# Optimization experiments

Measured on AMD Instinct MI355X. Metric: run time of the kernel, lower is better.

The kernel has to match this reference:

```python
import jax, jax.numpy as jnp
import numpy as np

B, S, D, H = 2, 2048, 2048, 16
HD = D // H
RESIDUAL_SCALE = 1.0
EPS = 1e-6


def setup_inputs() -> dict:
    key = jax.random.key(0)
    ks = jax.random.split(key, 6)
    x = jax.random.normal(ks[0], (B, S, D), jnp.float32)
    # rotary tables: emb = cat(freqs, freqs), shape [S, HD]
    inv_freq = 1.0 / (10000.0 ** (jnp.arange(0, HD, 2, dtype=jnp.float32) / HD))
    t = jnp.arange(S, dtype=jnp.float32)
    freqs = jnp.einsum('s,f->sf', t, inv_freq)
    emb = jnp.concatenate([freqs, freqs], axis=-1)
    cos, sin = jnp.cos(emb), jnp.sin(emb)
    sc = 0.02
    w_qkv = jax.random.normal(ks[1], (3 * D, D), jnp.float32) * sc
    w_out = jax.random.normal(ks[2], (D, D), jnp.float32) * sc
    w_fc1 = jax.random.normal(ks[3], (4 * D, D), jnp.float32) * sc
    w_fc2 = jax.random.normal(ks[4], (D, 4 * D), jnp.float32) * sc
    g1 = jnp.ones((D,), jnp.float32)
    g2 = jnp.ones((D,), jnp.float32)
    return {'x': x, 'cos': cos, 'sin': sin, 'g1': g1, 'g2': g2,
            'w_qkv': w_qkv, 'w_out': w_out, 'w_fc1': w_fc1, 'w_fc2': w_fc2}


def _rmsnorm(x, g):
    xf = x.astype(jnp.float32)
    norm = jnp.sqrt(jnp.mean(xf * xf, axis=-1, keepdims=True) + EPS)
    return g * (xf / norm)


def _rotate_half(x):
    x1, x2 = jnp.split(x, 2, axis=-1)
    return jnp.concatenate([-x2, x1], axis=-1)


def _rope(t, cos, sin):
    # t: [B, S, H, HD]; cos/sin: [S, HD]
    c = cos[None, :, None, :]
    s = sin[None, :, None, :]
    return t * c + _rotate_half(t) * s


def reference(x, cos, sin, g1, g2, w_qkv, w_out, w_fc1, w_fc2):
    b, s, d = x.shape
    x_skip = x
    h = _rmsnorm(x, g1)
    qkv = (h @ w_qkv.T).reshape(b, s, 3, H, HD)
    q = _rope(qkv[:, :, 0], cos, sin)
    k = _rope(qkv[:, :, 1], cos, sin)
    v = qkv[:, :, 2]  # rotary is identity on v
    scale = 1.0 / jnp.sqrt(jnp.asarray(HD, dtype=q.dtype))
    scores = jnp.einsum('bqhd,bkhd->bhqk', q, k) * scale
    causal = jnp.triu(jnp.ones((s, s), dtype=bool), k=1)
    scores = jnp.where(causal[None, None], -jnp.inf, scores)
    attn = jax.nn.softmax(scores, axis=-1)
    o = jnp.einsum('bhqk,bkhd->bqhd', attn, v).reshape(b, s, d)
    x = x_skip + RESIDUAL_SCALE * (o @ w_out.T)
    x_skip = x
    h = _rmsnorm(x, g2)
    h = jax.nn.gelu(h @ w_fc1.T, approximate=True) @ w_fc2.T
    return x_skip + RESIDUAL_SCALE * h
```

## Files before the change

kernel.cpp:

```cpp
#include <hip/hip_runtime.h>
#include <stdint.h>

typedef unsigned short u16;
typedef u16 u16x4 __attribute__((ext_vector_type(4)));
typedef u16 u16x8 __attribute__((ext_vector_type(8)));
typedef __bf16 bf16x8 __attribute__((ext_vector_type(8)));
typedef float f32x4 __attribute__((ext_vector_type(4)));
typedef float f32x16 __attribute__((ext_vector_type(16)));

#define MFMA16 __builtin_amdgcn_mfma_f32_16x16x32_bf16
#define MFMA32 __builtin_amdgcn_mfma_f32_32x32x16_bf16

static __device__ __forceinline__ float b2f(u16 u) {
    union { unsigned int i; float f; } v; v.i = ((unsigned int)u) << 16; return v.f;
}
static __device__ __forceinline__ u16 f2b(float f) {
    union { float f; unsigned int i; } v; v.f = f;
    unsigned int r = (v.i + 0x7fffu + ((v.i >> 16) & 1u)) >> 16;
    return (u16)r;
}
static __device__ __forceinline__ unsigned pk2(float lo, float hi) {
    union { __bf16 b[2]; unsigned u; } t;
    t.b[0] = (__bf16)lo; t.b[1] = (__bf16)hi; return t.u;
}
static __device__ __forceinline__ void gload_lds16(const void* g, void* l) {
    __builtin_amdgcn_global_load_lds((__attribute__((address_space(1))) void*)g,
                                     (__attribute__((address_space(3))) void*)l,
                                     16, 0, 0);
}

__global__ __launch_bounds__(256) void cvt4_k(const float* __restrict__ s0,
                                              const float* __restrict__ s1,
                                              const float* __restrict__ s2,
                                              const float* __restrict__ s3,
                                              u16* __restrict__ out) {
    long i = ((long)blockIdx.x * 256 + threadIdx.x) * 4;
    const float* src; long off;
    if (i < 12582912)      { src = s0; off = i; }
    else if (i < 16777216) { src = s1; off = i - 12582912; }
    else if (i < 33554432) { src = s2; off = i - 16777216; }
    else                   { src = s3; off = i - 33554432; }
    float4 v = *(const float4*)(src + off);
    u16x4 o; o[0] = f2b(v.x); o[1] = f2b(v.y); o[2] = f2b(v.z); o[3] = f2b(v.w);
    *(u16x4*)(out + i) = o;
}

__global__ __launch_bounds__(256) void addred_k(float* __restrict__ xout,
                                                const float* __restrict__ p0,
                                                const float* __restrict__ p1) {
    long i = ((long)blockIdx.x * 256 + threadIdx.x) * 4;
    float4 a = *(const float4*)(xout + i);
    float4 b = *(const float4*)(p0 + i);
    float4 c = *(const float4*)(p1 + i);
    a.x += b.x + c.x; a.y += b.y + c.y; a.z += b.z + c.z; a.w += b.w + c.w;
    *(float4*)(xout + i) = a;
}

__global__ __launch_bounds__(256) void addrednorm_k(float* xout,
                                                    const float* __restrict__ x,
                                                    const float* p0,
                                                    const float* __restrict__ p1,
                                                    const float* __restrict__ g,
                                                    u16* __restrict__ out) {
    const long row = blockIdx.x;
    const int tid = threadIdx.x;
    const long base = row * 2048;
    float4 a = *(const float4*)(x + base + tid * 4);
    float4 b = *(const float4*)(p0 + base + tid * 4);
    float4 c = *(const float4*)(p1 + base + tid * 4);
    a.x += b.x + c.x; a.y += b.y + c.y; a.z += b.z + c.z; a.w += b.w + c.w;
    float4 a2 = *(const float4*)(x + base + 1024 + tid * 4);
    float4 b2 = *(const float4*)(p0 + base + 1024 + tid * 4);
    float4 c2 = *(const float4*)(p1 + base + 1024 + tid * 4);
    a2.x += b2.x + c2.x; a2.y += b2.y + c2.y;
    a2.z += b2.z + c2.z; a2.w += b2.w + c2.w;
    *(float4*)(xout + base + tid * 4) = a;
    *(float4*)(xout + base + 1024 + tid * 4) = a2;
    float ss = a.x*a.x + a.y*a.y + a.z*a.z + a.w*a.w
             + a2.x*a2.x + a2.y*a2.y + a2.z*a2.z + a2.w*a2.w;
    #pragma unroll
    for (int d = 1; d < 64; d <<= 1) ss += __shfl_xor(ss, d);
    __shared__ float red[4];
    if ((tid & 63) == 0) red[tid >> 6] = ss;
    __syncthreads();
    float tot = red[0] + red[1] + red[2] + red[3];
    float rinv = rsqrtf(tot * (1.0f / 2048.0f) + 1e-6f);
    float4 g0 = *(const float4*)(g + tid * 4);
    float4 g1 = *(const float4*)(g + 1024 + tid * 4);
    u16x4 o0, o1;
    o0[0] = f2b(a.x * g0.x * rinv); o0[1] = f2b(a.y * g0.y * rinv);
    o0[2] = f2b(a.z * g0.z * rinv); o0[3] = f2b(a.w * g0.w * rinv);
    o1[0] = f2b(a2.x * g1.x * rinv); o1[1] = f2b(a2.y * g1.y * rinv);
    o1[2] = f2b(a2.z * g1.z * rinv); o1[3] = f2b(a2.w * g1.w * rinv);
    *(u16x4*)(out + base + tid * 4) = o0;
    *(u16x4*)(out + base + 1024 + tid * 4) = o1;
}

__global__ __launch_bounds__(256) void rmsnorm_k(const float* __restrict__ x,
                                                 const float* __restrict__ g,
                                                 u16* __restrict__ out) {
    const long row = blockIdx.x;
    const int tid = threadIdx.x;
    const float* xr = x + row * 2048;
    float4 a = *(const float4*)(xr + tid * 4);
    float4 b = *(const float4*)(xr + 1024 + tid * 4);
    float ss = a.x*a.x + a.y*a.y + a.z*a.z + a.w*a.w
             + b.x*b.x + b.y*b.y + b.z*b.z + b.w*b.w;
    #pragma unroll
    for (int d = 1; d < 64; d <<= 1) ss += __shfl_xor(ss, d);
    __shared__ float red[4];
    if ((tid & 63) == 0) red[tid >> 6] = ss;
    __syncthreads();
    float tot = red[0] + red[1] + red[2] + red[3];
    float rinv = rsqrtf(tot * (1.0f / 2048.0f) + 1e-6f);
    float4 g0 = *(const float4*)(g + tid * 4);
    float4 g1 = *(const float4*)(g + 1024 + tid * 4);
    u16x4 o0, o1;
    o0[0] = f2b(a.x * g0.x * rinv); o0[1] = f2b(a.y * g0.y * rinv);
    o0[2] = f2b(a.z * g0.z * rinv); o0[3] = f2b(a.w * g0.w * rinv);
    o1[0] = f2b(b.x * g1.x * rinv); o1[1] = f2b(b.y * g1.y * rinv);
    o1[2] = f2b(b.z * g1.z * rinv); o1[3] = f2b(b.w * g1.w * rinv);
    *(u16x4*)(out + row * 2048 + tid * 4) = o0;
    *(u16x4*)(out + row * 2048 + 1024 + tid * 4) = o1;
}

__global__ __launch_bounds__(256) void rope_k(u16* __restrict__ qkv,
                                              const float* __restrict__ cosb,
                                              const float* __restrict__ sinb) {
    long idx = (long)blockIdx.x * 256 + threadIdx.x;
    int d = (int)(idx & 15) * 4;
    int h = (int)((idx >> 4) & 15);
    int which = (int)((idx >> 8) & 1);
    long row = idx >> 9;
    int s = (int)(row & 2047);
    u16* base = qkv + row * 6144 + which * 2048 + h * 128;
    u16x4 ua = *(u16x4*)(base + d);
    u16x4 ub = *(u16x4*)(base + d + 64);
    float4 c4 = *(const float4*)(cosb + (long)s * 128 + d);
    float4 s4 = *(const float4*)(sinb + (long)s * 128 + d);
    float cc[4] = {c4.x, c4.y, c4.z, c4.w};
    float sn[4] = {s4.x, s4.y, s4.z, s4.w};
    float scale = (which == 0) ? 0.08838834764831845f : 1.0f;
    u16x4 oa, ob;
    #pragma unroll
    for (int j = 0; j < 4; ++j) {
        float a = b2f(ua[j]), b = b2f(ub[j]);
        oa[j] = f2b((a * cc[j] - b * sn[j]) * scale);
        ob[j] = f2b((b * cc[j] + a * sn[j]) * scale);
    }
    *(u16x4*)(base + d) = oa;
    *(u16x4*)(base + d + 64) = ob;
}

#define DS_A(BUF, SM) (*(const bf16x8*)(ldsb + (BUF)*16384 + ((SM) << 10) + rin64 + cst2))
#define DS_B(BUF, SN) (*(const bf16x8*)(ldsb + 32768 + (BUF)*16384 + ((SN) << 10) + rin64 + cst2))
#define STAGE_A(BUF, KT) do { \
    gload_lds16(sA0 + ((long)(KT)*32), ldsb + (BUF)*16384 + (w*2)*1024); \
    gload_lds16(sA1 + ((long)(KT)*32), ldsb + (BUF)*16384 + (w*2+1)*1024); \
} while (0)
#define STAGE_B(BUF, KT) do { \
    gload_lds16(sB0 + ((long)(KT)*32), ldsb + 32768 + (BUF)*16384 + (w*2)*1024); \
    gload_lds16(sB1 + ((long)(KT)*32), ldsb + 32768 + (BUF)*16384 + (w*2+1)*1024); \
} while (0)
#define PREF_A(DST, BUF, MH) do { \
    _Pragma("unroll") \
    for (int m = 0; m < 4; ++m) DST[m] = DS_A(BUF, wr8 + (MH)*4 + m); \
} while (0)
#define PREF_B(DST, BUF) do { \
    _Pragma("unroll") \
    for (int n = 0; n < 4; ++n) DST[n] = DS_B(BUF, wc4 + n); \
} while (0)
#define MFMA_Q(MH, AF, BF) do { \
    _Pragma("unroll") \
    for (int m = 0; m < 4; ++m) \
        _Pragma("unroll") \
        for (int n = 0; n < 4; ++n) \
            acc[(MH)*4 + m][n] = MFMA16(AF[m], BF[n], acc[(MH)*4 + m][n], 0, 0, 0); \
} while (0)
#define VMC2 asm volatile("s_waitcnt vmcnt(2)" ::: "memory")
#define BAR  __builtin_amdgcn_s_barrier()

template <int EPI>
__global__ __launch_bounds__(512, 2) void gemm256(const u16* __restrict__ A,
                                                  const u16* __restrict__ W,
                                                  int M, int N, int K,
                                                  u16* outb, float* outf,
                                                  float* outf2, const float* res,
                                                  u16* vtw, int ksplit) {
    __shared__ u16 lds_[32768];
    char* ldsb = (char*)lds_;
    const int tid = threadIdx.x;
    const int w = tid >> 6, l = tid & 63;
    const int wr8 = (w >> 2) * 8;
    const int wc4 = (w & 3) * 4;
    const int rin64 = (l & 15) * 64;
    const int cst2 = ((((l >> 4) * 8) ^ (((l >> 3) & 1) << 4)) << 1);

    const int nbn = N >> 8;
    const int nbm = M >> 8;
    const int nwg = gridDim.x;
    const int cpx = nwg >> 3;
    const int bid = blockIdx.x;
    int wg = (bid & 7) * cpx + (bid >> 3);
    int kseg = 0;
    int Keff = K;
    if (ksplit == 2) {
        kseg = wg & 1;
        wg >>= 1;
        Keff = K >> 1;
    }
    const int grp = 8 * nbn;
    const int g8 = wg / grp;
    const int rem = wg - g8 * grp;
    const int bm0 = g8 * 8;
    const int gmh = (nbm - bm0 < 8) ? (nbm - bm0) : 8;
    const int bn = rem / gmh;
    const int bm = bm0 + rem % gmh;
    const u16* Ab = A + (long)kseg * Keff;
    const u16* Wb = W + (long)kseg * Keff;

    const int r4 = l >> 2;
    const int clog = ((l & 3) * 8) ^ (((r4 >> 3) & 1) << 4);
    const u16* sA0 = Ab + ((long)bm * 256 + (w * 2 + 0) * 16 + r4) * K + clog;
    const u16* sA1 = Ab + ((long)bm * 256 + (w * 2 + 1) * 16 + r4) * K + clog;
    const u16* sB0 = Wb + ((long)bn * 256 + (w * 2 + 0) * 16 + r4) * K + clog;
    const u16* sB1 = Wb + ((long)bn * 256 + (w * 2 + 1) * 16 + r4) * K + clog;

    f32x4 acc[8][4];
    #pragma unroll
    for (int m = 0; m < 8; ++m)
        #pragma unroll
        for (int n = 0; n < 4; ++n) acc[m][n] = (f32x4){0.f, 0.f, 0.f, 0.f};
    bf16x8 afc[4], afn[4], bfc[4], bfn[4];

    const int nkt = Keff >> 5;
    const int niter = nkt >> 1;

    STAGE_A(0, 0); STAGE_B(0, 0); STAGE_A(1, 1); STAGE_B(1, 1);
    asm volatile("s_waitcnt vmcnt(4)" ::: "memory");
    BAR;
    PREF_A(afc, 0, 0); PREF_B(bfc, 0);
    BAR;

    for (int it = 0; it < niter; ++it) {
        const int t = it * 2;
        const int t2 = (t + 2 < nkt) ? t + 2 : nkt - 1;
        const int t3 = (t + 3 < nkt) ? t + 3 : nkt - 1;
        PREF_A(afn, 0, 1);
        STAGE_B(0, t2);
        MFMA_Q(0, afc, bfc);
        VMC2;
        BAR;
        PREF_A(afc, 1, 0); PREF_B(bfn, 1);
        STAGE_A(0, t2);
        MFMA_Q(1, afn, bfc);
        BAR;
        PREF_A(afn, 1, 1);
        STAGE_B(1, t3);
        MFMA_Q(0, afc, bfn);
        VMC2;
        BAR;
        PREF_A(afc, 0, 0); PREF_B(bfc, 0);
        STAGE_A(1, t3);
        MFMA_Q(1, afn, bfn);
        BAR;
    }
    asm volatile("s_waitcnt vmcnt(0)" ::: "memory");

    const int rb = bm * 256 + (wr8 >> 3) * 128 + ((l >> 4) << 2);
    const int cb = bn * 256 + (w & 3) * 64 + (l & 15);
    if (EPI == 4) {
        const bool vreg = (cb >= 4096);
        #pragma unroll
        for (int m = 0; m < 8; ++m) {
            long row0 = rb + m * 16;
            #pragma unroll
            for (int n = 0; n < 4; ++n) {
                long col = cb + n * 16;
                if (vreg) {
                    int d = (int)col & 127;
                    int hh = ((int)col >> 7) - 32;
                    long bh = (row0 >> 11) * 16 + hh;
                    int s = (int)(row0 & 2047);
                    u16x4 o4;
                    #pragma unroll
                    for (int r = 0; r < 4; ++r) o4[r] = f2b(acc[m][n][r]);
                    *(u16x4*)(vtw + (bh * 128 + d) * 2048 + s) = o4;
                } else {
                    #pragma unroll
                    for (int r = 0; r < 4; ++r)
                        outb[(row0 + r) * N + col] = f2b(acc[m][n][r]);
                }
            }
        }
        return;
    }
    float* pf = (EPI == 3) ? (kseg ? outf2 : outf) : outf;
    #pragma unroll
    for (int m = 0; m < 8; ++m) {
        #pragma unroll
        for (int r = 0; r < 4; ++r) {
            long row = rb + m * 16 + r;
            #pragma unroll
            for (int n = 0; n < 4; ++n) {
                long col = cb + n * 16;
                float v = acc[m][n][r];
                if (EPI == 1) {
                    pf[row * N + col] = res[row * N + col] + v;
                } else if (EPI == 2) {
                    float u = 0.7978845608028654f * v * (1.0f + 0.044715f * v * v);
                    float e = __expf(2.0f * u);
                    float tgl = 1.0f - 2.0f / (e + 1.0f);
                    outb[row * N + col] = f2b(0.5f * v * (1.0f + tgl));
                } else if (EPI == 3) {
                    pf[row * N + col] = v;
                } else {
                    outb[row * N + col] = f2b(v);
                }
            }
        }
    }
}

struct AttnState {
    f32x16 acc[4];
    float m_i, l_i;
};

template <bool DIAG>
static __device__ __forceinline__ void attn_tile(
    int kv0, int qg, bool do_g1, int l31, int hi,
    const u16* __restrict__ Ks, const u16* __restrict__ Vt,
    const bf16x8 (&qf)[8], AttnState& st)
{
    f32x16 sacc0, sacc1;
    #pragma unroll
    for (int r = 0; r < 16; ++r) { sacc0[r] = 0.f; sacc1[r] = 0.f; }

    __builtin_amdgcn_s_setprio(1);
    #pragma unroll
    for (int dsl = 0; dsl < 8; ++dsl) {
        int slot = dsl * 2 + hi;
        int kv = l31;
        int sw = (slot & 8) | ((slot & 7) ^ (kv & 7));
        bf16x8 kf = *(const bf16x8*)(Ks + kv * 128 + sw * 8);
        sacc0 = MFMA32(kf, qf[dsl], sacc0, 0, 0, 0);
    }
    if (do_g1) {
        #pragma unroll
        for (int dsl = 0; dsl < 8; ++dsl) {
            int slot = dsl * 2 + hi;
            int kv = 32 + l31;
            int sw = (slot & 8) | ((slot & 7) ^ (kv & 7));
            bf16x8 kf = *(const bf16x8*)(Ks + kv * 128 + sw * 8);
            sacc1 = MFMA32(kf, qf[dsl], sacc1, 0, 0, 0);
        }
    }
    __builtin_amdgcn_s_setprio(0);

    float sv[2][16];
    #pragma unroll
    for (int r = 0; r < 16; ++r) {
        sv[0][r] = sacc0[r];
        sv[1][r] = do_g1 ? sacc1[r] : -INFINITY;
    }
    if (DIAG) {
        #pragma unroll
        for (int g = 0; g < 2; ++g)
            #pragma unroll
            for (int r = 0; r < 16; ++r) {
                int kvg = kv0 + g * 32 + ((r & 3) + 8 * (r >> 2) + 4 * hi);
                if (kvg > qg) sv[g][r] = -INFINITY;
            }
    }

    float mx = sv[0][0];
    #pragma unroll
    for (int r = 1; r < 16; ++r) mx = fmaxf(mx, sv[0][r]);
    #pragma unroll
    for (int r = 0; r < 16; ++r) mx = fmaxf(mx, sv[1][r]);
    mx = fmaxf(mx, __shfl_xor(mx, 32));

    bool defer = __all(mx <= st.m_i + 8.0f);
    if (!defer) {
        float mnew = fmaxf(st.m_i, mx);
        float f = __expf(st.m_i - mnew);
        st.l_i *= f;
        #pragma unroll
        for (int dblk = 0; dblk < 4; ++dblk)
            #pragma unroll
            for (int r = 0; r < 16; ++r) st.acc[dblk][r] *= f;
        st.m_i = mnew;
    }

    float ssum = 0.f;
    #pragma unroll
    for (int g = 0; g < 2; ++g)
        #pragma unroll
        for (int r = 0; r < 16; ++r) {
            float e = __expf(sv[g][r] - st.m_i);
            sv[g][r] = e;
            ssum += e;
        }
    ssum += __shfl_xor(ssum, 32);
    st.l_i += ssum;

    unsigned w[2][4][2];
    #pragma unroll
    for (int g = 0; g < 2; ++g)
        #pragma unroll
        for (int q4 = 0; q4 < 4; ++q4) {
            w[g][q4][0] = pk2(sv[g][4 * q4 + 0], sv[g][4 * q4 + 1]);
            w[g][q4][1] = pk2(sv[g][4 * q4 + 2], sv[g][4 * q4 + 3]);
        }
    bf16x8 pfrag[4];
    #pragma unroll
    for (int ks = 0; ks < 4; ++ks) {
        int g = ks >> 1, h2 = ks & 1;
        unsigned o0 = hi ? w[g][2 * h2 + 1][0] : w[g][2 * h2][0];
        unsigned o1 = hi ? w[g][2 * h2 + 1][1] : w[g][2 * h2][1];
        unsigned t0 = hi ? w[g][2 * h2][0] : w[g][2 * h2 + 1][0];
        unsigned t1 = hi ? w[g][2 * h2][1] : w[g][2 * h2 + 1][1];
        unsigned s0v = __shfl_xor(t0, 32);
        unsigned s1v = __shfl_xor(t1, 32);
        union { unsigned u[4]; bf16x8 v; } cv;
        cv.u[0] = hi ? s0v : o0;
        cv.u[1] = hi ? s1v : o1;
        cv.u[2] = hi ? o0 : s0v;
        cv.u[3] = hi ? o1 : s1v;
        pfrag[ks] = cv.v;
    }

    __builtin_amdgcn_s_setprio(1);
    #pragma unroll
    for (int dblk = 0; dblk < 4; ++dblk) {
        int d = dblk * 32 + l31;
        #pragma unroll
        for (int ks = 0; ks < 4; ++ks) {
            if (ks >= 2 && !do_g1) continue;
            int slot = ks * 2 + hi;
            bf16x8 vf = *(const bf16x8*)(Vt + d * 64 + (slot ^ (d & 7)) * 8);
            st.acc[dblk] = MFMA32(vf, pfrag[ks], st.acc[dblk], 0, 0, 0);
        }
    }
    __builtin_amdgcn_s_setprio(0);
}

__global__ __launch_bounds__(512) void attn5_k(const u16* __restrict__ qkv,
                                               const u16* __restrict__ vt,
                                               u16* __restrict__ out) {
    const int bh = blockIdx.y;
    const int b = bh >> 4, h = bh & 15;
    const int j = blockIdx.x;
    const int tid = threadIdx.x, wave = tid >> 6, lane = tid & 63;
    const int l31 = lane & 31, hi = lane >> 5;
    const int brow = b * 2048;
    __shared__ u16 Ks_lds[2][64 * 128];
    __shared__ u16 Vt_lds[2][128 * 64];

    const int tsel = wave >> 1;
    const int qt = (tsel == 0) ? j : (tsel == 1) ? (15 - j)
                 : (tsel == 2) ? (16 + j) : (31 - j);
    const int r0 = qt * 64 + (wave & 1) * 32;
    const int qg = r0 + l31;

    bf16x8 qf[8];
    {
        const u16* qp = qkv + (long)(brow + r0 + l31) * 6144 + h * 128 + hi * 8;
        #pragma unroll
        for (int dsl = 0; dsl < 8; ++dsl) qf[dsl] = *(const bf16x8*)(qp + dsl * 16);
    }

    AttnState st;
    st.m_i = -INFINITY; st.l_i = 0.f;
    #pragma unroll
    for (int dblk = 0; dblk < 4; ++dblk)
        #pragma unroll
        for (int r = 0; r < 16; ++r) st.acc[dblk][r] = 0.f;

    const int nt = 32 - j;
    int cur = 0;

    const int krow = tid >> 4;
    const int kslot = tid & 15;
    const int vrow = tid >> 3;
    const int vslot = tid & 7;

#define STAGE_KV(BUF, KV0) do { \
    _Pragma("unroll") \
    for (int i = 0; i < 2; ++i) { \
        int kv = i * 32 + krow; \
        int sw = (kslot & 8) | ((kslot & 7) ^ (kv & 7)); \
        const u16* src = qkv + (long)(brow + (KV0) + kv) * 6144 + 2048 + \
                         h * 128 + sw * 8; \
        gload_lds16(src, (char*)Ks_lds[BUF] + (i * 32 + wave * 4) * 256); \
    } \
    _Pragma("unroll") \
    for (int i = 0; i < 2; ++i) { \
        int d = i * 64 + vrow; \
        int sw = vslot ^ (d & 7); \
        const u16* src = vt + ((long)bh * 128 + d) * 2048 + (KV0) + sw * 8; \
        gload_lds16(src, (char*)Vt_lds[BUF] + (i * 64 + wave * 8) * 128); \
    } \
} while (0)

    STAGE_KV(0, 0);
    for (int t = 0; t < nt; ++t) {
        const int kv0 = t * 64;
        const bool more = (t + 1 < nt);
        if (more) {
            if (cur) STAGE_KV(0, kv0 + 64); else STAGE_KV(1, kv0 + 64);
        }
        if (more) { asm volatile("s_waitcnt vmcnt(4)" ::: "memory"); }
        else      { asm volatile("s_waitcnt vmcnt(0)" ::: "memory"); }
        __builtin_amdgcn_sched_barrier(0);
        __builtin_amdgcn_s_barrier();
        __builtin_amdgcn_sched_barrier(0);
        {
            const u16* Ks = Ks_lds[cur];
            const u16* Vt_ = Vt_lds[cur];
            const int delta = r0 - kv0;
            if (delta >= 64)
                attn_tile<false>(kv0, qg, true, l31, hi, Ks, Vt_, qf, st);
            else if (delta >= 0)
                attn_tile<true>(kv0, qg, delta >= 32, l31, hi, Ks, Vt_, qf, st);
        }
        __builtin_amdgcn_sched_barrier(0);
        __builtin_amdgcn_s_barrier();
        __builtin_amdgcn_sched_barrier(0);
        cur ^= 1;
    }
#undef STAGE_KV

    float inv = 1.0f / st.l_i;
    long orow = (long)(brow + r0 + l31);
    #pragma unroll
    for (int dblk = 0; dblk < 4; ++dblk)
        #pragma unroll
        for (int rq = 0; rq < 4; ++rq) {
            u16x4 o4;
            #pragma unroll
            for (int m = 0; m < 4; ++m) o4[m] = f2b(st.acc[dblk][rq * 4 + m] * inv);
            int d = dblk * 32 + 8 * rq + 4 * hi;
            *(u16x4*)(out + orow * 2048 + h * 128 + d) = o4;
        }
}

extern "C" void kernel_launch(void* const* d_in, const int* in_sizes, int n_in,
                              void* d_out, int out_size, void* d_ws, size_t ws_size,
                              hipStream_t stream) {
    const float* x     = (const float*)d_in[0];
    const float* cosb  = (const float*)d_in[1];
    const float* sinb  = (const float*)d_in[2];
    const float* g1    = (const float*)d_in[3];
    const float* g2    = (const float*)d_in[4];
    const float* w_qkv = (const float*)d_in[5];
    const float* w_out = (const float*)d_in[6];
    const float* w_fc1 = (const float*)d_in[7];
    const float* w_fc2 = (const float*)d_in[8];

    char* ws = (char*)d_ws;
    u16* wqkv_b = (u16*)(ws);
    u16* wout_b = (u16*)(ws + 25165824);
    u16* wfc1_b = (u16*)(ws + 33554432);
    u16* wfc2_b = (u16*)(ws + 67108864);
    u16* h_b    = (u16*)(ws + 100663296);
    u16* qkv_b  = (u16*)(ws + 117440512);
    u16* attn_b = (u16*)(ws + 167772160);
    u16* hg_b   = qkv_b;
    u16* vt_b   = (u16*)d_out;
    float* p0op = (float*)d_out;
    float* p1op = (float*)(ws + 117440512);
    float* part = (float*)ws;
    float* xout = (float*)d_out;

    cvt4_k<<<49152, 256, 0, stream>>>(w_qkv, w_out, w_fc1, w_fc2, (u16*)ws);

    rmsnorm_k<<<4096, 256, 0, stream>>>(x, g1, h_b);
    gemm256<4><<<384, 512, 0, stream>>>(h_b, wqkv_b, 4096, 6144, 2048,
                                        qkv_b, nullptr, nullptr, nullptr,
                                        vt_b, 1);
    rope_k<<<8192, 256, 0, stream>>>(qkv_b, cosb, sinb);
    attn5_k<<<dim3(8, 32), 512, 0, stream>>>(qkv_b, vt_b, attn_b);
    gemm256<3><<<256, 512, 0, stream>>>(attn_b, wout_b, 4096, 2048, 2048,
                                        nullptr, p0op, p1op, nullptr,
                                        nullptr, 2);
    addrednorm_k<<<4096, 256, 0, stream>>>(xout, x, p0op, p1op, g2, h_b);
    gemm256<2><<<512, 512, 0, stream>>>(h_b, wfc1_b, 4096, 8192, 2048,
                                        hg_b, nullptr, nullptr, nullptr,
                                        nullptr, 1);
    gemm256<3><<<256, 512, 0, stream>>>(hg_b, wfc2_b, 4096, 2048, 8192,
                                        nullptr, part, part + 8388608, nullptr,
                                        nullptr, 2);
    addred_k<<<8192, 256, 0, stream>>>(xout, part, part + 8388608);
}
```

Before: 573.7 us.

## Split-K by four with bf16 partials for out-proj and fc2 GEMMs

The out-projection and fc2 GEMMs now split K four ways instead of two, launching 512 workgroups instead of 256 to fill more CUs. Each split writes its partial sums as bf16 rather than fp32, and the reduction kernels sum four bf16 partials. MFMA bursts are wrapped in s_setprio to favour matrix issue. In exchange, the bf16 partials lose precision before accumulation, and the extra splits add reduction traffic. The out-proj partials reuse the h_b buffer region.

```diff
diff --git a/kernel.cpp b/kernel.cpp
--- a/kernel.cpp
+++ b/kernel.cpp
@@ -28,6 +28,8 @@
                                      (__attribute__((address_space(3))) void*)l,
                                      16, 0, 0);
 }
+
+#define MNQ 8388608L
 
 __global__ __launch_bounds__(256) void cvt4_k(const float* __restrict__ s0,
                                               const float* __restrict__ s1,
@@ -45,37 +47,40 @@
     *(u16x4*)(out + i) = o;
 }
 
-__global__ __launch_bounds__(256) void addred_k(float* __restrict__ xout,
-                                                const float* __restrict__ p0,
-                                                const float* __restrict__ p1) {
+__global__ __launch_bounds__(256) void addred4b_k(float* __restrict__ xout,
+                                                  const u16* __restrict__ p) {
     long i = ((long)blockIdx.x * 256 + threadIdx.x) * 4;
     float4 a = *(const float4*)(xout + i);
-    float4 b = *(const float4*)(p0 + i);
-    float4 c = *(const float4*)(p1 + i);
-    a.x += b.x + c.x; a.y += b.y + c.y; a.z += b.z + c.z; a.w += b.w + c.w;
+    #pragma unroll
+    for (int k = 0; k < 4; ++k) {
+        u16x4 v = *(const u16x4*)(p + k * MNQ + i);
+        a.x += b2f(v[0]); a.y += b2f(v[1]); a.z += b2f(v[2]); a.w += b2f(v[3]);
+    }
     *(float4*)(xout + i) = a;
 }
 
-__global__ __launch_bounds__(256) void addrednorm_k(float* xout,
-                                                    const float* __restrict__ x,
-                                                    const float* p0,
-                                                    const float* __restrict__ p1,
-                                                    const float* __restrict__ g,
-                                                    u16* __restrict__ out) {
+__global__ __launch_bounds__(256) void addrednorm4b_k(float* __restrict__ xout,
+                                                      const float* __restrict__ x,
+                                                      const u16* p,
+                                                      const float* __restrict__ g,
+                                                      u16* outh) {
     const long row = blockIdx.x;
     const int tid = threadIdx.x;
     const long base = row * 2048;
-    float4 a = *(const float4*)(x + base + tid * 4);
-    float4 b = *(const float4*)(p0 + base + tid * 4);
-    float4 c = *(const float4*)(p1 + base + tid * 4);
-    a.x += b.x + c.x; a.y += b.y + c.y; a.z += b.z + c.z; a.w += b.w + c.w;
-    float4 a2 = *(const float4*)(x + base + 1024 + tid * 4);
-    float4 b2 = *(const float4*)(p0 + base + 1024 + tid * 4);
-    float4 c2 = *(const float4*)(p1 + base + 1024 + tid * 4);
-    a2.x += b2.x + c2.x; a2.y += b2.y + c2.y;
-    a2.z += b2.z + c2.z; a2.w += b2.w + c2.w;
-    *(float4*)(xout + base + tid * 4) = a;
-    *(float4*)(xout + base + 1024 + tid * 4) = a2;
+    const long i0 = base + tid * 4;
+    const long i1 = base + 1024 + tid * 4;
+    float4 a = *(const float4*)(x + i0);
+    float4 a2 = *(const float4*)(x + i1);
+    #pragma unroll
+    for (int k = 0; k < 4; ++k) {
+        u16x4 v = *(const u16x4*)(p + k * MNQ + i0);
+        a.x += b2f(v[0]); a.y += b2f(v[1]); a.z += b2f(v[2]); a.w += b2f(v[3]);
+        u16x4 v2 = *(const u16x4*)(p + k * MNQ + i1);
+        a2.x += b2f(v2[0]); a2.y += b2f(v2[1]);
+        a2.z += b2f(v2[2]); a2.w += b2f(v2[3]);
+    }
+    *(float4*)(xout + i0) = a;
+    *(float4*)(xout + i1) = a2;
     float ss = a.x*a.x + a.y*a.y + a.z*a.z + a.w*a.w
              + a2.x*a2.x + a2.y*a2.y + a2.z*a2.z + a2.w*a2.w;
     #pragma unroll
@@ -92,8 +97,8 @@
     o0[2] = f2b(a.z * g0.z * rinv); o0[3] = f2b(a.w * g0.w * rinv);
     o1[0] = f2b(a2.x * g1.x * rinv); o1[1] = f2b(a2.y * g1.y * rinv);
     o1[2] = f2b(a2.z * g1.z * rinv); o1[3] = f2b(a2.w * g1.w * rinv);
-    *(u16x4*)(out + base + tid * 4) = o0;
-    *(u16x4*)(out + base + 1024 + tid * 4) = o1;
+    *(u16x4*)(outh + i0) = o0;
+    *(u16x4*)(outh + i1) = o1;
 }
 
 __global__ __launch_bounds__(256) void rmsnorm_k(const float* __restrict__ x,
@@ -171,11 +176,13 @@
     for (int n = 0; n < 4; ++n) DST[n] = DS_B(BUF, wc4 + n); \
 } while (0)
 #define MFMA_Q(MH, AF, BF) do { \
+    __builtin_amdgcn_s_setprio(1); \
     _Pragma("unroll") \
     for (int m = 0; m < 4; ++m) \
         _Pragma("unroll") \
         for (int n = 0; n < 4; ++n) \
             acc[(MH)*4 + m][n] = MFMA16(AF[m], BF[n], acc[(MH)*4 + m][n], 0, 0, 0); \
+    __builtin_amdgcn_s_setprio(0); \
 } while (0)
 #define VMC2 asm volatile("s_waitcnt vmcnt(2)" ::: "memory")
 #define BAR  __builtin_amdgcn_s_barrier()
@@ -185,8 +192,8 @@
                                                   const u16* __restrict__ W,
                                                   int M, int N, int K,
                                                   u16* outb, float* outf,
-                                                  float* outf2, const float* res,
-                                                  u16* vtw, int ksplit) {
+                                                  const float* res, u16* vtw,
+                                                  u16* pq, int ksplit) {
     __shared__ u16 lds_[32768];
     char* ldsb = (char*)lds_;
     const int tid = threadIdx.x;
@@ -204,10 +211,10 @@
     int wg = (bid & 7) * cpx + (bid >> 3);
     int kseg = 0;
     int Keff = K;
-    if (ksplit == 2) {
-        kseg = wg & 1;
-        wg >>= 1;
-        Keff = K >> 1;
+    if (ksplit == 4) {
+        kseg = wg & 3;
+        wg >>= 2;
+        Keff = K >> 2;
     }
     const int grp = 8 * nbn;
     const int g8 = wg / grp;
@@ -295,7 +302,20 @@
         }
         return;
     }
-    float* pf = (EPI == 3) ? (kseg ? outf2 : outf) : outf;
+    if (EPI == 6) {
+        u16* pb = pq + (long)kseg * MNQ;
+        #pragma unroll
+        for (int m = 0; m < 8; ++m) {
+            #pragma unroll
+            for (int r = 0; r < 4; ++r) {
+                long row = rb + m * 16 + r;
+                #pragma unroll
+                for (int n = 0; n < 4; ++n)
+                    pb[row * N + cb + n * 16] = f2b(acc[m][n][r]);
+            }
+        }
+        return;
+    }
     #pragma unroll
     for (int m = 0; m < 8; ++m) {
         #pragma unroll
@@ -306,14 +326,12 @@
                 long col = cb + n * 16;
                 float v = acc[m][n][r];
                 if (EPI == 1) {
-                    pf[row * N + col] = res[row * N + col] + v;
+                    outf[row * N + col] = res[row * N + col] + v;
                 } else if (EPI == 2) {
                     float u = 0.7978845608028654f * v * (1.0f + 0.044715f * v * v);
                     float e = __expf(2.0f * u);
                     float tgl = 1.0f - 2.0f / (e + 1.0f);
                     outb[row * N + col] = f2b(0.5f * v * (1.0f + tgl));
-                } else if (EPI == 3) {
-                    pf[row * N + col] = v;
                 } else {
                     outb[row * N + col] = f2b(v);
                 }
@@ -569,28 +587,27 @@
     u16* attn_b = (u16*)(ws + 167772160);
     u16* hg_b   = qkv_b;
     u16* vt_b   = (u16*)d_out;
-    float* p0op = (float*)d_out;
-    float* p1op = (float*)(ws + 117440512);
-    float* part = (float*)ws;
+    u16* pop  = h_b;
+    u16* pfc2 = (u16*)ws;
     float* xout = (float*)d_out;
 
     cvt4_k<<<49152, 256, 0, stream>>>(w_qkv, w_out, w_fc1, w_fc2, (u16*)ws);
 
     rmsnorm_k<<<4096, 256, 0, stream>>>(x, g1, h_b);
     gemm256<4><<<384, 512, 0, stream>>>(h_b, wqkv_b, 4096, 6144, 2048,
-                                        qkv_b, nullptr, nullptr, nullptr,
-                                        vt_b, 1);
+                                        qkv_b, nullptr, nullptr, vt_b,
+                                        nullptr, 1);
     rope_k<<<8192, 256, 0, stream>>>(qkv_b, cosb, sinb);
     attn5_k<<<dim3(8, 32), 512, 0, stream>>>(qkv_b, vt_b, attn_b);
-    gemm256<3><<<256, 512, 0, stream>>>(attn_b, wout_b, 4096, 2048, 2048,
-                                        nullptr, p0op, p1op, nullptr,
-                                        nullptr, 2);
-    addrednorm_k<<<4096, 256, 0, stream>>>(xout, x, p0op, p1op, g2, h_b);
+    gemm256<6><<<512, 512, 0, stream>>>(attn_b, wout_b, 4096, 2048, 2048,
+                                        nullptr, nullptr, nullptr, nullptr,
+                                        pop, 4);
+    addrednorm4b_k<<<4096, 256, 0, stream>>>(xout, x, pop, g2, h_b);
     gemm256<2><<<512, 512, 0, stream>>>(h_b, wfc1_b, 4096, 8192, 2048,
                                         hg_b, nullptr, nullptr, nullptr,
                                         nullptr, 1);
-    gemm256<3><<<256, 512, 0, stream>>>(hg_b, wfc2_b, 4096, 2048, 8192,
-                                        nullptr, part, part + 8388608, nullptr,
-                                        nullptr, 2);
-    addred_k<<<8192, 256, 0, stream>>>(xout, part, part + 8388608);
-}
+    gemm256<6><<<512, 512, 0, stream>>>(hg_b, wfc2_b, 4096, 2048, 8192,
+                                        nullptr, nullptr, nullptr, nullptr,
+                                        pfc2, 4);
+    addred4b_k<<<8192, 256, 0, stream>>>(xout, pfc2);
+}
```

After: 587.9 us. +2.5%, slower.
